# Kernel optimization log

Hardware: AMD Instinct MI355X
Metric: run time of the kernel (lower is better)

## Reference

```python
import jax, jax.numpy as jnp
import numpy as np

N = 100000      # nodes
E = 500000      # edges
F_IN = 165      # Elliptic feature dim
HID = 128       # hidden
HEADS = 2
DH = HID // HEADS  # 64, per-head GAT out dim
EPS = 1e-5


def setup_inputs() -> dict:
    key = jax.random.key(0)
    ks = jax.random.split(key, 40)

    def w(k, shape, fan_in):
        return (jax.random.normal(k, shape, jnp.float32) / np.sqrt(fan_in)).astype(jnp.float32)

    def bn_params(k, d):
        k1, k2 = jax.random.split(k)
        return (jnp.ones((d,), jnp.float32),                       # gamma
                jnp.zeros((d,), jnp.float32),                      # beta
                0.1 * jax.random.normal(k1, (d,), jnp.float32),    # running mean
                jax.random.uniform(k2, (d,), jnp.float32, 0.5, 1.5))  # running var

    bn1 = bn_params(ks[10], HID)
    bn2 = bn_params(ks[11], HID)
    bn3 = bn_params(ks[12], DH)

    return {
        "x": jax.random.normal(ks[0], (N, F_IN), jnp.float32),
        "edge_index": jax.random.randint(ks[1], (2, E), 0, N, jnp.int32),
        # input_proj
        "w_in": w(ks[2], (F_IN, HID), F_IN), "b_in": jnp.zeros((HID,), jnp.float32),
        # GCNConv
        "w_gcn": w(ks[3], (HID, HID), HID), "b_gcn": jnp.zeros((HID,), jnp.float32),
        "bn1_g": bn1[0], "bn1_b": bn1[1], "bn1_m": bn1[2], "bn1_v": bn1[3],
        # GATConv (heads=2, out=64, concat)
        "w_gat": w(ks[4], (HID, HEADS * DH), HID),
        "att_src": 0.1 * jax.random.normal(ks[5], (HEADS, DH), jnp.float32),
        "att_dst": 0.1 * jax.random.normal(ks[6], (HEADS, DH), jnp.float32),
        "b_gat": jnp.zeros((HEADS * DH,), jnp.float32),
        "bn2_g": bn2[0], "bn2_b": bn2[1], "bn2_m": bn2[2], "bn2_v": bn2[3],
        # SAGEConv (mean aggr)
        "w_sage_l": w(ks[7], (HID, DH), HID), "b_sage": jnp.zeros((DH,), jnp.float32),
        "w_sage_r": w(ks[8], (HID, DH), HID),
        "bn3_g": bn3[0], "bn3_b": bn3[1], "bn3_m": bn3[2], "bn3_v": bn3[3],
        # residual proj + classifier
        "w_res": w(ks[9], (HID, DH), HID), "b_res": jnp.zeros((DH,), jnp.float32),
        "w_c1": w(ks[13], (DH, 32), DH), "b_c1": jnp.zeros((32,), jnp.float32),
        "w_c2": w(ks[14], (32, 2), 32), "b_c2": jnp.zeros((2,), jnp.float32),
    }


def _bn(h, g, b, m, v):
    # eval-mode BatchNorm1d with running stats
    return (h - m) * (g / jnp.sqrt(v + EPS)) + b


def reference(x, edge_index, w_in, b_in, w_gcn, b_gcn,
              bn1_g, bn1_b, bn1_m, bn1_v,
              w_gat, att_src, att_dst, b_gat,
              bn2_g, bn2_b, bn2_m, bn2_v,
              w_sage_l, b_sage, w_sage_r,
              bn3_g, bn3_b, bn3_m, bn3_v,
              w_res, b_res, w_c1, b_c1, w_c2, b_c2):
    n = x.shape[0]
    src, dst = edge_index[0], edge_index[1]
    loop = jnp.arange(n, dtype=src.dtype)
    src_l = jnp.concatenate([src, loop])   # edges + self loops (GCN & GAT)
    dst_l = jnp.concatenate([dst, loop])

    # ---- input_proj (dropout = identity in eval) ----
    h = jax.nn.elu(x @ w_in + b_in)
    residual = h

    hw = h @ w_gcn
    deg = jax.ops.segment_sum(jnp.ones_like(dst_l, jnp.float32), dst_l, n)
    dinv = jnp.where(deg > 0, jax.lax.rsqrt(deg), 0.0)
    norm = dinv[src_l] * dinv[dst_l]                      # [E+N]
    h1 = jax.ops.segment_sum(hw[src_l] * norm[:, None], dst_l, n) + b_gcn
    h1 = jax.nn.elu(_bn(h1, bn1_g, bn1_b, bn1_m, bn1_v))

    # ---- GATConv (heads=2, concat, self loops, leaky_relu 0.2) ----
    g = (h1 @ w_gat).reshape(n, HEADS, DH)
    a_src = jnp.sum(g * att_src, axis=-1)                 # [N, H]
    a_dst = jnp.sum(g * att_dst, axis=-1)
    e = jax.nn.leaky_relu(a_src[src_l] + a_dst[dst_l], 0.2)   # [E+N, H]
    mx = jax.ops.segment_max(e, dst_l, n)                 # per-dst softmax max
    ex = jnp.exp(e - mx[dst_l])
    denom = jax.ops.segment_sum(ex, dst_l, n)
    alpha = ex / (denom[dst_l] + 1e-16)                   # [E+N, H]
    h2 = jax.ops.segment_sum(g[src_l] * alpha[:, :, None], dst_l, n)
    h2 = h2.reshape(n, HEADS * DH) + b_gat
    h2 = jax.nn.elu(_bn(h2, bn2_g, bn2_b, bn2_m, bn2_v))

    # ---- SAGEConv: W_l mean(neighbors) + W_r x + b (no self loops) ----
    deg_s = jax.ops.segment_sum(jnp.ones_like(dst, jnp.float32), dst, n)
    mean_nb = jax.ops.segment_sum(h2[src], dst, n) / jnp.maximum(deg_s, 1.0)[:, None]
    h3 = mean_nb @ w_sage_l + b_sage + h2 @ w_sage_r
    h3 = _bn(h3, bn3_g, bn3_b, bn3_m, bn3_v)
    h3 = jax.nn.elu(h3 + residual @ w_res + b_res)

    # ---- classifier ----
    z = jax.nn.elu(h3 @ w_c1 + b_c1)
    return z @ w_c2 + b_c2
```

## Files before the change

kernel.cpp:

```cpp
#include <hip/hip_runtime.h>
#include <cstdint>
#include <cstddef>

#define BN_EPS 1e-5f

typedef __attribute__((ext_vector_type(8))) short short8v;
typedef __attribute__((ext_vector_type(4))) float float4v;
typedef __attribute__((ext_vector_type(4))) unsigned int uint4v;
typedef unsigned int uint32;
typedef unsigned short ushort16;

__device__ __forceinline__ float elu_f(float v){ return v > 0.f ? v : expm1f(v); }
__device__ __forceinline__ float leaky_f(float v){ return v > 0.f ? v : 0.2f*v; }
__device__ __forceinline__ uint32 f2bf(float f){
  uint32 b = __float_as_uint(f);
  return (b + 0x7fffu + ((b >> 16) & 1u)) >> 16;
}
__device__ __forceinline__ float bflo(uint32 u){ return __uint_as_float(u << 16); }
__device__ __forceinline__ float bfhi(uint32 u){ return __uint_as_float(u & 0xffff0000u); }
__device__ __forceinline__ float readlane_f(float v, int l){
  return __int_as_float(__builtin_amdgcn_readlane(__float_as_int(v), l));
}
__device__ __forceinline__ uint32 fenc(float f){
  uint32 u = __float_as_uint(f);
  return (u >> 31) ? ~u : (u | 0x80000000u);
}
__device__ __forceinline__ float fdec(uint32 e){
  return (e & 0x80000000u) ? __uint_as_float(e & 0x7fffffffu) : __uint_as_float(~e);
}


__global__ void count_deg_kernel(const int* __restrict__ dst, int E, int* __restrict__ cnt){
  int i = blockIdx.x*blockDim.x + threadIdx.x;
  if(i < E) atomicAdd(&cnt[dst[i]], 1);
}

__global__ __launch_bounds__(1024) void scan_blocks(const int* __restrict__ cnt, int n,
                                                    int* __restrict__ part, int* __restrict__ bsum){
  __shared__ int wsum[16];
  int tid = threadIdx.x, lane = tid & 63, w = tid >> 6;
  int i = blockIdx.x*1024 + tid;
  int v = (i < n) ? cnt[i] : 0;
  int sv = v;
#pragma unroll
  for(int o = 1; o < 64; o <<= 1){
    int u = __shfl_up(sv, o);
    if(lane >= o) sv += u;
  }
  if(lane == 63) wsum[w] = sv;
  __syncthreads();
  int woff = 0;
#pragma unroll
  for(int q = 0; q < 16; q++) woff += (q < w) ? wsum[q] : 0;
  if(i < n) part[i] = woff + sv - v;
  if(tid == 1023) bsum[blockIdx.x] = woff + sv;
}

__global__ __launch_bounds__(1024) void scan_bsum(const int* __restrict__ bsum, int nb,
                                                  int* __restrict__ boff, int* __restrict__ rowptr, int n){
  __shared__ int wsum[16];
  int tid = threadIdx.x, lane = tid & 63, w = tid >> 6;
  int v = (tid < nb) ? bsum[tid] : 0;
  int sv = v;
#pragma unroll
  for(int o = 1; o < 64; o <<= 1){
    int u = __shfl_up(sv, o);
    if(lane >= o) sv += u;
  }
  if(lane == 63) wsum[w] = sv;
  __syncthreads();
  int woff = 0;
#pragma unroll
  for(int q = 0; q < 16; q++) woff += (q < w) ? wsum[q] : 0;
  if(tid < nb) boff[tid] = woff + sv - v;
  if(tid == 1023) rowptr[n] = woff + sv;
}

__global__ void scan_add_dinv(const int* __restrict__ part, const int* __restrict__ boff,
                              const int* __restrict__ cnt, int n,
                              int* __restrict__ rowptr, float* __restrict__ dinv){
  int i = blockIdx.x*blockDim.x + threadIdx.x;
  if(i < n){
    rowptr[i] = part[i] + boff[i >> 10];
    dinv[i] = rsqrtf((float)cnt[i] + 1.0f);
  }
}

__global__ void scatter_kernel(const int* __restrict__ src, const int* __restrict__ dst, int E,
                               const int* __restrict__ rowptr, int* __restrict__ fill,
                               int* __restrict__ col, int* __restrict__ pos){
  int i = blockIdx.x*blockDim.x + threadIdx.x;
  if(i < E){
    int s = src[i], d = dst[i];
    int p = rowptr[d] + atomicAdd(&fill[d], 1);
    col[p] = s;
    pos[i] = p;
  }
}


__global__ __launch_bounds__(256) void cvt_x(const float* __restrict__ x, uint2* __restrict__ xb, int total){
  int idx = blockIdx.x*256 + threadIdx.x;
  if(idx >= total) return;
  int row = idx/48;
  int cp = idx - row*48;
  int c = cp*4;
  const float* xr = x + (size_t)row*165;
  float v0 = (c   < 165) ? xr[c]   : 0.f;
  float v1 = (c+1 < 165) ? xr[c+1] : 0.f;
  float v2 = (c+2 < 165) ? xr[c+2] : 0.f;
  float v3 = (c+3 < 165) ? xr[c+3] : 0.f;
  xb[idx] = make_uint2(f2bf(v0) | (f2bf(v1) << 16), f2bf(v2) | (f2bf(v3) << 16));
}


__global__ void prep_scales(const float* __restrict__ bn1_g, const float* __restrict__ bn1_b,
    const float* __restrict__ bn1_m, const float* __restrict__ bn1_v, const float* __restrict__ b_gcn,
    const float* __restrict__ bn2_g, const float* __restrict__ bn2_b,
    const float* __restrict__ bn2_m, const float* __restrict__ bn2_v, const float* __restrict__ b_gat,
    const float* __restrict__ att_s, const float* __restrict__ att_d,
    const float* __restrict__ bn3_g, const float* __restrict__ bn3_b,
    const float* __restrict__ bn3_m, const float* __restrict__ bn3_v,
    const float* __restrict__ b_sage, const float* __restrict__ b_res,
    float* __restrict__ s1, float* __restrict__ b1c,
    float* __restrict__ s2, float* __restrict__ b2c,
    float* __restrict__ atts2, float* __restrict__ attd2,
    float* __restrict__ s3, float* __restrict__ bias3){
  int c = threadIdx.x;
  float v1 = bn1_g[c]*rsqrtf(bn1_v[c] + BN_EPS);
  s1[c] = v1;
  b1c[c] = (b_gcn[c] - bn1_m[c])*v1 + bn1_b[c];
  float v2 = bn2_g[c]*rsqrtf(bn2_v[c] + BN_EPS);
  s2[c] = v2;
  b2c[c] = (b_gat[c] - bn2_m[c])*v2 + bn2_b[c];
  atts2[c] = att_s[c]/v2;
  attd2[c] = att_d[c]/v2;
  if(c < 64){
    float v3 = bn3_g[c]*rsqrtf(bn3_v[c] + BN_EPS);
    s3[c] = v3;
    bias3[c] = (b_sage[c] - bn3_m[c])*v3 + bn3_b[c] + b_res[c];
  }
}


__device__ __forceinline__ void pack_region(const float* __restrict__ W, int K, int NOUT, int kbase, int idx,
                                            const float* __restrict__ scale, ushort16* __restrict__ out){
  int k = idx / NOUT, c = idx - k*NOUT;
  float v = (k < K) ? W[(size_t)k*NOUT + c] : 0.f;
  if(scale) v *= scale[c];
  int pk = kbase + k;
  out[(size_t)(pk >> 3)*NOUT*8 + (size_t)c*8 + (pk & 7)] = (ushort16)f2bf(v);
}

__global__ __launch_bounds__(256) void pack_all(const float* __restrict__ w_in, const float* __restrict__ w_gcn,
    const float* __restrict__ w_gat, const float* __restrict__ w_sl, const float* __restrict__ w_sr,
    const float* __restrict__ w_res,
    const float* __restrict__ s1, const float* __restrict__ s2, const float* __restrict__ s3,
    ushort16* __restrict__ pw_in, ushort16* __restrict__ pw_gcn,
    ushort16* __restrict__ pw_gat, ushort16* __restrict__ pw_cat){
  int b = blockIdx.x, t = threadIdx.x;
  if(b < 96)       pack_region(w_in,  165, 128, 0,   b*256 + t,        nullptr, pw_in);
  else if(b < 160) pack_region(w_gcn, 128, 128, 0,   (b-96)*256 + t,   s1,      pw_gcn);
  else if(b < 224) pack_region(w_gat, 128, 128, 0,   (b-160)*256 + t,  s2,      pw_gat);
  else if(b < 256) pack_region(w_sl,  128, 64,  0,   (b-224)*256 + t,  s3,      pw_cat);
  else if(b < 288) pack_region(w_sr,  128, 64,  128, (b-256)*256 + t,  s3,      pw_cat);
  else             pack_region(w_res, 128, 64,  256, (b-288)*256 + t,  nullptr, pw_cat);
}


template<int KSTEPS, int NOUT, int EPI>
__global__ __launch_bounds__(256) void mfma_gemm(
    const ushort16* __restrict__ A, int lda,
    const uint4v* __restrict__ pw,
    const float* __restrict__ bias,
    void* __restrict__ out, int ldo, int N,
    const float* __restrict__ dinv,
    const float* __restrict__ atts2, const float* __restrict__ attd2,
    float* __restrict__ a_src, float* __restrict__ a_dst,
    float* __restrict__ ess, uint32* __restrict__ Mint)
{
  constexpr int LDSV = KSTEPS*4*NOUT;
  __shared__ uint4v wlds[LDSV];
  int t = threadIdx.x;
#pragma unroll
  for(int q = 0; q < LDSV/256; q++)
    wlds[q*256 + t] = pw[q*256 + t];
  __syncthreads();

  int wid = t >> 6, lane = t & 63;
  int wm, wn;
  if(NOUT == 128){ wm = wid >> 1; wn = wid & 1; } else { wm = wid; wn = 0; }
  constexpr int MTILE = (NOUT == 128) ? 128 : 256;
  long row0 = (long)blockIdx.x*MTILE + wm*64;
  int l15 = lane & 15, lk = lane >> 4;
  int wn64 = wn*64;
  const ushort16* wl = (const ushort16*)wlds;

  float4v acc[4][4];
#pragma unroll
  for(int fm = 0; fm < 4; fm++)
#pragma unroll
    for(int fn = 0; fn < 4; fn++) acc[fm][fn] = (float4v){0.f,0.f,0.f,0.f};

  const ushort16* abase[4];
#pragma unroll
  for(int fm = 0; fm < 4; fm++){
    long r = row0 + fm*16 + l15;
    if(r > (long)N - 1) r = (long)N - 1;
    abase[fm] = A + r*(size_t)lda + lk*8;
  }

  short8v a[4];
#pragma unroll
  for(int fm = 0; fm < 4; fm++) a[fm] = *(const short8v*)(abase[fm]);

#pragma unroll
  for(int ks = 0; ks < KSTEPS; ks++){
    short8v b[4];
#pragma unroll
    for(int fn = 0; fn < 4; fn++){
      int c = wn64 + fn*16 + l15;
      b[fn] = *(const short8v*)(wl + ((size_t)((ks*4 + lk)*NOUT + c))*8);
    }
    short8v an[4];
    if(ks + 1 < KSTEPS){
#pragma unroll
      for(int fm = 0; fm < 4; fm++) an[fm] = *(const short8v*)(abase[fm] + (ks + 1)*32);
    }
#pragma unroll
    for(int fm = 0; fm < 4; fm++)
#pragma unroll
      for(int fn = 0; fn < 4; fn++)
        acc[fm][fn] = __builtin_amdgcn_mfma_f32_16x16x32_bf16(a[fm], b[fn], acc[fm][fn], 0, 0, 0);
    if(ks + 1 < KSTEPS){
#pragma unroll
      for(int fm = 0; fm < 4; fm++) a[fm] = an[fm];
    }
  }

#pragma unroll
  for(int fm = 0; fm < 4; fm++){
#pragma unroll
    for(int rr = 0; rr < 4; rr++){
      long r = row0 + fm*16 + lk*4 + rr;
      if(r < N){
        float dr = 0.f;
        if constexpr(EPI == 4) dr = dinv[r];
#pragma unroll
        for(int fn = 0; fn < 4; fn++){
          int c = wn64 + fn*16 + l15;
          float v = acc[fm][fn][rr];
          if constexpr(EPI == 1){ v += bias[c]; v = elu_f(v); }
          if constexpr(EPI == 4){ v *= dr; }
          ((ushort16*)out)[r*(size_t)ldo + c] = (ushort16)f2bf(v);
        }
      }
    }
  }

  if constexpr(EPI == 3){
    float as2[4], ad2[4];
#pragma unroll
    for(int fn = 0; fn < 4; fn++){
      int c = wn64 + fn*16 + l15;
      as2[fn] = atts2[c]; ad2[fn] = attd2[c];
    }
#pragma unroll
    for(int fm = 0; fm < 4; fm++){
#pragma unroll
      for(int rr = 0; rr < 4; rr++){
        float p1 = 0.f, p2 = 0.f;
#pragma unroll
        for(int fn = 0; fn < 4; fn++){
          p1 += acc[fm][fn][rr]*as2[fn];
          p2 += acc[fm][fn][rr]*ad2[fn];
        }
#pragma unroll
        for(int o = 1; o < 16; o <<= 1){
          p1 += __shfl_xor(p1, o);
          p2 += __shfl_xor(p2, o);
        }
        long r = row0 + fm*16 + lk*4 + rr;
        if(l15 == 0 && r < N){
          a_src[2*r + wn] = p1;
          a_dst[2*r + wn] = p2;
          float es = leaky_f(p1 + p2);
          ess[2*r + wn] = es;
          Mint[2*r + wn] = fenc(es);
        }
      }
    }
  }
}


__global__ __launch_bounds__(256) void gcn_agg(const uint32* __restrict__ hw2,
    const int* __restrict__ rowptr, const int* __restrict__ col,
    const float* __restrict__ dinv, const float* __restrict__ b1c,
    uint32* __restrict__ h1, int N)
{
  int t = threadIdx.x & 63;
  int w = __builtin_amdgcn_readfirstlane(threadIdx.x >> 6);
  float2 bc = ((const float2*)b1c)[t];
  int stride = gridDim.x*4;
  for(int i = blockIdx.x*4 + w; i < N; i += stride){
    int beg = rowptr[i], end = rowptr[i+1];
    float di = dinv[i];
    uint32 su = hw2[(size_t)i*64 + t];
    float a0 = bflo(su), a1 = bfhi(su);
#define GCN_ROW(q) { int row = __builtin_amdgcn_readlane(s, q); \
    uint32 u = hw2[(size_t)row*64 + t]; a0 += bflo(u); a1 += bfhi(u); }
    for(int c0 = beg; c0 < end; c0 += 64){
      int p = c0 + t;
      int cl = end - c0; if(cl > 64) cl = 64;
      int s = (p < end) ? col[p] : 0;
      int q = 0;
      for(; q + 4 <= cl; q += 4){ GCN_ROW(q) GCN_ROW(q+1) GCN_ROW(q+2) GCN_ROW(q+3) }
      for(; q < cl; q++){ GCN_ROW(q) }
    }
#undef GCN_ROW
    float v0 = a0*di + bc.x;
    float v1 = a1*di + bc.y;
    h1[(size_t)i*64 + t] = f2bf(elu_f(v0)) | (f2bf(elu_f(v1)) << 16);
  }
}


__global__ void edge_logit(const int* __restrict__ src, const int* __restrict__ dst,
                           const int* __restrict__ pos, int E,
                           const float* __restrict__ a_src, const float* __restrict__ a_dst,
                           float2* __restrict__ lcsr, uint32* __restrict__ Mint){
  int i = blockIdx.x*blockDim.x + threadIdx.x;
  if(i >= E) return;
  int s = src[i], d = dst[i], p = pos[i];
  float2 as = ((const float2*)a_src)[s];
  float2 ad = ((const float2*)a_dst)[d];
  float l0 = leaky_f(as.x + ad.x);
  float l1 = leaky_f(as.y + ad.y);
  lcsr[p] = make_float2(l0, l1);
  atomicMax(&Mint[2*d],   fenc(l0));
  atomicMax(&Mint[2*d+1], fenc(l1));
}


__global__ __launch_bounds__(256) void gat_gather(const uint32* __restrict__ g,
    const int* __restrict__ rowptr, const int* __restrict__ col,
    const float2* __restrict__ lcsr, const uint32* __restrict__ Mint, const float* __restrict__ ess,
    const float* __restrict__ b2c, uint32* __restrict__ h2out, int N)
{
  int t = threadIdx.x & 63;
  int w = __builtin_amdgcn_readfirstlane(threadIdx.x >> 6);
  float2 bc = ((const float2*)b2c)[t];
  int hl = t >> 5;
  int stride = gridDim.x*4;
  for(int i = blockIdx.x*4 + w; i < N; i += stride){
    int beg = rowptr[i], end = rowptr[i+1];
    float M0 = fdec(Mint[2*i]), M1 = fdec(Mint[2*i+1]);
    float es0 = ess[2*i], es1 = ess[2*i+1];
    float d0 = 0.f, d1 = 0.f, a0 = 0.f, a1 = 0.f;
#define GAT_ROW(q) { int row = __builtin_amdgcn_readlane(s, q); \
    float w0q = readlane_f(e0, q); \
    float w1q = readlane_f(e1, q); \
    float wq = hl ? w1q : w0q; \
    uint32 u = g[(size_t)row*64 + t]; a0 += wq*bflo(u); a1 += wq*bfhi(u); }
    for(int c0 = beg; c0 < end; c0 += 64){
      int p = c0 + t;
      int cl = end - c0; if(cl > 64) cl = 64;
      float e0 = 0.f, e1 = 0.f; int s = 0;
      if(p < end){
        float2 l = lcsr[p];
        e0 = __expf(l.x - M0); e1 = __expf(l.y - M1);
        s = col[p];
      }
      d0 += e0; d1 += e1;
      int q = 0;
      for(; q + 4 <= cl; q += 4){ GAT_ROW(q) GAT_ROW(q+1) GAT_ROW(q+2) GAT_ROW(q+3) }
      for(; q < cl; q++){ GAT_ROW(q) }
    }
#undef GAT_ROW
#pragma unroll
    for(int o = 32; o > 0; o >>= 1){ d0 += __shfl_xor(d0, o); d1 += __shfl_xor(d1, o); }
    float sw0 = __expf(es0 - M0), sw1 = __expf(es1 - M1);
    float rD = 1.f/(((hl ? d1 : d0) + (hl ? sw1 : sw0)) + 1e-16f);
    float sw = hl ? sw1 : sw0;
    uint32 su = g[(size_t)i*64 + t];
    float v0 = (a0 + sw*bflo(su))*rD + bc.x;
    float v1 = (a1 + sw*bfhi(su))*rD + bc.y;
    h2out[(size_t)i*192 + t] = f2bf(elu_f(v0)) | (f2bf(elu_f(v1)) << 16);
  }
}


__global__ __launch_bounds__(256) void sage_mean(const uint32* __restrict__ h2,
    const int* __restrict__ rowptr, const int* __restrict__ col,
    uint32* __restrict__ mout, int N)
{
  int t = threadIdx.x & 63;
  int w = __builtin_amdgcn_readfirstlane(threadIdx.x >> 6);
  int stride = gridDim.x*4;
  for(int i = blockIdx.x*4 + w; i < N; i += stride){
    int beg = rowptr[i], end = rowptr[i+1];
    float a0 = 0.f, a1 = 0.f;
#define SAGE_ROW(q) { int row = __builtin_amdgcn_readlane(s, q); \
    uint32 u = h2[(size_t)row*192 + t]; a0 += bflo(u); a1 += bfhi(u); }
    for(int c0 = beg; c0 < end; c0 += 64){
      int p = c0 + t;
      int cl = end - c0; if(cl > 64) cl = 64;
      int s = (p < end) ? col[p] : 0;
      int q = 0;
      for(; q + 4 <= cl; q += 4){ SAGE_ROW(q) SAGE_ROW(q+1) SAGE_ROW(q+2) SAGE_ROW(q+3) }
      for(; q < cl; q++){ SAGE_ROW(q) }
    }
#undef SAGE_ROW
    float inv = 1.f/fmaxf((float)(end - beg), 1.f);
    mout[(size_t)i*192 + t] = f2bf(a0*inv) | (f2bf(a1*inv) << 16);
  }
}


__global__ __launch_bounds__(256) void classifier_kernel(const uint32* __restrict__ h3,
    const float* __restrict__ w1, const float* __restrict__ b1,
    const float* __restrict__ w2, const float* __restrict__ b2,
    float* __restrict__ out, int N)
{
  __shared__ float hs[8][64];
  __shared__ float zs[8][32];
  int node0 = blockIdx.x*8;
  int t = threadIdx.x;
  {
    int r = t >> 5, cp = t & 31;
    int nd = node0 + r;
    uint32 u = (nd < N) ? h3[(size_t)nd*32 + cp] : 0u;
    hs[r][2*cp]   = bflo(u);
    hs[r][2*cp+1] = bfhi(u);
  }
  __syncthreads();
  int nn = t >> 5, ln = t & 31;
  float acc = b1[ln];
#pragma unroll
  for(int k = 0; k < 64; k++) acc += hs[nn][k]*w1[k*32 + ln];
  zs[nn][ln] = elu_f(acc);
  __syncthreads();
  int node = node0 + nn;
  if(ln < 2 && node < N){
    float o = b2[ln];
#pragma unroll
    for(int k = 0; k < 32; k++) o += zs[nn][k]*w2[k*2 + ln];
    out[(size_t)node*2 + ln] = o;
  }
}


extern "C" void kernel_launch(void* const* d_in, const int* in_sizes, int n_in,
                              void* d_out, int out_size, void* d_ws, size_t ws_size,
                              hipStream_t stream)
{
  (void)n_in; (void)out_size; (void)ws_size;
  const float* x      = (const float*)d_in[0];
  const int*   ei     = (const int*)  d_in[1];
  const float* w_in   = (const float*)d_in[2];
  const float* b_in   = (const float*)d_in[3];
  const float* w_gcn  = (const float*)d_in[4];
  const float* b_gcn  = (const float*)d_in[5];
  const float* bn1_g  = (const float*)d_in[6];
  const float* bn1_b  = (const float*)d_in[7];
  const float* bn1_m  = (const float*)d_in[8];
  const float* bn1_v  = (const float*)d_in[9];
  const float* w_gat  = (const float*)d_in[10];
  const float* att_s  = (const float*)d_in[11];
  const float* att_d  = (const float*)d_in[12];
  const float* b_gat  = (const float*)d_in[13];
  const float* bn2_g  = (const float*)d_in[14];
  const float* bn2_b  = (const float*)d_in[15];
  const float* bn2_m  = (const float*)d_in[16];
  const float* bn2_v  = (const float*)d_in[17];
  const float* w_sl   = (const float*)d_in[18];
  const float* b_sage = (const float*)d_in[19];
  const float* w_sr   = (const float*)d_in[20];
  const float* bn3_g  = (const float*)d_in[21];
  const float* bn3_b  = (const float*)d_in[22];
  const float* bn3_m  = (const float*)d_in[23];
  const float* bn3_v  = (const float*)d_in[24];
  const float* w_res  = (const float*)d_in[25];
  const float* b_res  = (const float*)d_in[26];
  const float* w_c1   = (const float*)d_in[27];
  const float* b_c1   = (const float*)d_in[28];
  const float* w_c2   = (const float*)d_in[29];
  const float* b_c2   = (const float*)d_in[30];

  const int F_IN = 165;
  int N = in_sizes[0]/F_IN;
  int E = in_sizes[1]/2;
  const int* srcp = ei;
  const int* dstp = ei + E;
  int nb = (N + 1023) >> 10;

  char* p = (char*)d_ws;
  auto alloc = [&](size_t bytes) -> char* {
    char* q = p; p += (bytes + 255) & ~(size_t)255; return q;
  };
  ushort16* Acat  = (ushort16*)alloc((size_t)N*384*2);
  ushort16* xb    = (ushort16*)alloc((size_t)N*192*2);
  ushort16* bufG  = (ushort16*)alloc((size_t)N*128*2);
  float* a_src    = (float*)alloc((size_t)N*2*4);
  float* a_dst    = (float*)alloc((size_t)N*2*4);
  float* ess      = (float*)alloc((size_t)N*2*4);
  uint32* Mint    = (uint32*)alloc((size_t)N*2*4);
  float* dinv     = (float*)alloc((size_t)N*4);
  int* cnt        = (int*)alloc((size_t)N*4);
  int* fill       = (int*)alloc((size_t)N*4);
  int* rowptr     = (int*)alloc((size_t)(N+1)*4);
  int* part       = (int*)alloc((size_t)N*4);
  int* bsum       = (int*)alloc(1024*4);
  int* boff       = (int*)alloc(1024*4);
  int* col        = (int*)alloc((size_t)E*4);
  int* pos        = (int*)alloc((size_t)E*4);
  float2* lcsr    = (float2*)alloc((size_t)E*8);
  float* s1       = (float*)alloc(128*4);
  float* b1c      = (float*)alloc(128*4);
  float* s2       = (float*)alloc(128*4);
  float* b2c      = (float*)alloc(128*4);
  float* atts2    = (float*)alloc(128*4);
  float* attd2    = (float*)alloc(128*4);
  float* s3       = (float*)alloc(64*4);
  float* bias3    = (float*)alloc(64*4);
  ushort16* pw_in  = (ushort16*)alloc(6*4*128*16);
  ushort16* pw_gcn = (ushort16*)alloc(4*4*128*16);
  ushort16* pw_gat = (ushort16*)alloc(4*4*128*16);
  ushort16* pw_cat = (ushort16*)alloc(12*4*64*16);

  ushort16* h1 = xb;
  ushort16* h3 = bufG;

  hipMemsetAsync(cnt, 0, (size_t)((char*)(fill + N) - (char*)cnt), stream);

  count_deg_kernel<<<(E+255)/256, 256, 0, stream>>>(dstp, E, cnt);
  scan_blocks<<<nb, 1024, 0, stream>>>(cnt, N, part, bsum);
  scan_bsum<<<1, 1024, 0, stream>>>(bsum, nb, boff, rowptr, N);
  scan_add_dinv<<<(N+255)/256, 256, 0, stream>>>(part, boff, cnt, N, rowptr, dinv);
  scatter_kernel<<<(E+255)/256, 256, 0, stream>>>(srcp, dstp, E, rowptr, fill, col, pos);

  cvt_x<<<(N*48 + 255)/256, 256, 0, stream>>>(x, (uint2*)xb, N*48);
  prep_scales<<<1, 128, 0, stream>>>(bn1_g, bn1_b, bn1_m, bn1_v, b_gcn,
                                     bn2_g, bn2_b, bn2_m, bn2_v, b_gat,
                                     att_s, att_d,
                                     bn3_g, bn3_b, bn3_m, bn3_v, b_sage, b_res,
                                     s1, b1c, s2, b2c, atts2, attd2, s3, bias3);
  pack_all<<<320, 256, 0, stream>>>(w_in, w_gcn, w_gat, w_sl, w_sr, w_res,
                                    s1, s2, s3, pw_in, pw_gcn, pw_gat, pw_cat);

  int g128 = (N + 127)/128;
  int g256 = (N + 255)/256;
  int gagg = (N + 3)/4; if(gagg > 4096) gagg = 4096;

  mfma_gemm<6,128,1><<<g128, 256, 0, stream>>>(xb, 192, (const uint4v*)pw_in, b_in,
      (void*)(Acat + 256), 384, N, nullptr, nullptr, nullptr, nullptr, nullptr, nullptr, nullptr);
  mfma_gemm<4,128,4><<<g128, 256, 0, stream>>>(Acat + 256, 384, (const uint4v*)pw_gcn, nullptr,
      (void*)bufG, 128, N, dinv, nullptr, nullptr, nullptr, nullptr, nullptr, nullptr);
  gcn_agg<<<gagg, 256, 0, stream>>>((const uint32*)bufG, rowptr, col, dinv, b1c,
                                    (uint32*)h1, N);
  mfma_gemm<4,128,3><<<g128, 256, 0, stream>>>(h1, 128, (const uint4v*)pw_gat, nullptr,
      (void*)bufG, 128, N, nullptr, atts2, attd2, a_src, a_dst, ess, Mint);
  edge_logit<<<(E+255)/256, 256, 0, stream>>>(srcp, dstp, pos, E, a_src, a_dst, lcsr, Mint);
  gat_gather<<<gagg, 256, 0, stream>>>((const uint32*)bufG, rowptr, col, lcsr, Mint, ess,
                                       b2c, (uint32*)Acat + 64, N);
  sage_mean<<<gagg, 256, 0, stream>>>((const uint32*)Acat + 64, rowptr, col, (uint32*)Acat, N);
  mfma_gemm<12,64,1><<<g256, 256, 0, stream>>>(Acat, 384, (const uint4v*)pw_cat, bias3,
      (void*)h3, 64, N, nullptr, nullptr, nullptr, nullptr, nullptr, nullptr, nullptr);
  classifier_kernel<<<(N+7)/8, 256, 0, stream>>>((const uint32*)h3, w_c1, b_c1, w_c2, b_c2,
                                                 (float*)d_out, N);
}
```

Measured before the change: 378.3 us.

## Fuse GAT edge logits and softmax max into the gather kernel

Removes the separate edge_logit kernel, along with its pos/lcsr buffers and the atomicMax on encoded per-node maxima. The gather kernel now computes leaky-relu logits per edge from a_src/a_dst and takes the softmax max with a wave-level shuffle reduction. Rows with degree up to 64 do this in one pass. Larger rows make a second pass over col and a_src to recompute the logits. This saves an E-sized kernel launch, its scattered writes and its atomics, and the scatter kernel no longer writes pos, at the cost of extra gathers of a_src inside the aggregation.

```diff
diff --git a/kernel.cpp b/kernel.cpp
--- a/kernel.cpp
+++ b/kernel.cpp
@@ -20,13 +20,6 @@
 __device__ __forceinline__ float bfhi(uint32 u){ return __uint_as_float(u & 0xffff0000u); }
 __device__ __forceinline__ float readlane_f(float v, int l){
   return __int_as_float(__builtin_amdgcn_readlane(__float_as_int(v), l));
-}
-__device__ __forceinline__ uint32 fenc(float f){
-  uint32 u = __float_as_uint(f);
-  return (u >> 31) ? ~u : (u | 0x80000000u);
-}
-__device__ __forceinline__ float fdec(uint32 e){
-  return (e & 0x80000000u) ? __uint_as_float(e & 0x7fffffffu) : __uint_as_float(~e);
 }
 
 
@@ -88,13 +81,12 @@
 
 __global__ void scatter_kernel(const int* __restrict__ src, const int* __restrict__ dst, int E,
                                const int* __restrict__ rowptr, int* __restrict__ fill,
-                               int* __restrict__ col, int* __restrict__ pos){
+                               int* __restrict__ col){
   int i = blockIdx.x*blockDim.x + threadIdx.x;
   if(i < E){
     int s = src[i], d = dst[i];
     int p = rowptr[d] + atomicAdd(&fill[d], 1);
     col[p] = s;
-    pos[i] = p;
   }
 }
 
@@ -177,7 +169,7 @@
     const float* __restrict__ dinv,
     const float* __restrict__ atts2, const float* __restrict__ attd2,
     float* __restrict__ a_src, float* __restrict__ a_dst,
-    float* __restrict__ ess, uint32* __restrict__ Mint)
+    float* __restrict__ ess)
 {
   constexpr int LDSV = KSTEPS*4*NOUT;
   __shared__ uint4v wlds[LDSV];
@@ -284,9 +276,7 @@
         if(l15 == 0 && r < N){
           a_src[2*r + wn] = p1;
           a_dst[2*r + wn] = p2;
-          float es = leaky_f(p1 + p2);
-          ess[2*r + wn] = es;
-          Mint[2*r + wn] = fenc(es);
+          ess[2*r + wn] = leaky_f(p1 + p2);
         }
       }
     }
@@ -326,27 +316,11 @@
 }
 
 
-__global__ void edge_logit(const int* __restrict__ src, const int* __restrict__ dst,
-                           const int* __restrict__ pos, int E,
-                           const float* __restrict__ a_src, const float* __restrict__ a_dst,
-                           float2* __restrict__ lcsr, uint32* __restrict__ Mint){
-  int i = blockIdx.x*blockDim.x + threadIdx.x;
-  if(i >= E) return;
-  int s = src[i], d = dst[i], p = pos[i];
-  float2 as = ((const float2*)a_src)[s];
-  float2 ad = ((const float2*)a_dst)[d];
-  float l0 = leaky_f(as.x + ad.x);
-  float l1 = leaky_f(as.y + ad.y);
-  lcsr[p] = make_float2(l0, l1);
-  atomicMax(&Mint[2*d],   fenc(l0));
-  atomicMax(&Mint[2*d+1], fenc(l1));
-}
-
-
 __global__ __launch_bounds__(256) void gat_gather(const uint32* __restrict__ g,
     const int* __restrict__ rowptr, const int* __restrict__ col,
-    const float2* __restrict__ lcsr, const uint32* __restrict__ Mint, const float* __restrict__ ess,
-    const float* __restrict__ b2c, uint32* __restrict__ h2out, int N)
+    const float* __restrict__ a_src, const float* __restrict__ a_dst,
+    const float* __restrict__ ess, const float* __restrict__ b2c,
+    uint32* __restrict__ h2out, int N)
 {
   int t = threadIdx.x & 63;
   int w = __builtin_amdgcn_readfirstlane(threadIdx.x >> 6);
@@ -355,29 +329,62 @@
   int stride = gridDim.x*4;
   for(int i = blockIdx.x*4 + w; i < N; i += stride){
     int beg = rowptr[i], end = rowptr[i+1];
-    float M0 = fdec(Mint[2*i]), M1 = fdec(Mint[2*i+1]);
+    int deg = end - beg;
+    float2 ad = ((const float2*)a_dst)[i];
     float es0 = ess[2*i], es1 = ess[2*i+1];
     float d0 = 0.f, d1 = 0.f, a0 = 0.f, a1 = 0.f;
-#define GAT_ROW(q) { int row = __builtin_amdgcn_readlane(s, q); \
+    float M0, M1;
+#define GAT_ROWF(q) { int row = __builtin_amdgcn_readlane(s, q); \
     float w0q = readlane_f(e0, q); \
     float w1q = readlane_f(e1, q); \
     float wq = hl ? w1q : w0q; \
     uint32 u = g[(size_t)row*64 + t]; a0 += wq*bflo(u); a1 += wq*bfhi(u); }
-    for(int c0 = beg; c0 < end; c0 += 64){
-      int p = c0 + t;
-      int cl = end - c0; if(cl > 64) cl = 64;
-      float e0 = 0.f, e1 = 0.f; int s = 0;
+    if(deg <= 64){
+      int p = beg + t;
+      int s = 0; float l0 = -3e38f, l1 = -3e38f;
       if(p < end){
-        float2 l = lcsr[p];
-        e0 = __expf(l.x - M0); e1 = __expf(l.y - M1);
         s = col[p];
+        float2 as = ((const float2*)a_src)[s];
+        l0 = leaky_f(as.x + ad.x);
+        l1 = leaky_f(as.y + ad.y);
       }
-      d0 += e0; d1 += e1;
+      float m0 = fmaxf(l0, es0), m1 = fmaxf(l1, es1);
+#pragma unroll
+      for(int o = 32; o > 0; o >>= 1){ m0 = fmaxf(m0, __shfl_xor(m0, o)); m1 = fmaxf(m1, __shfl_xor(m1, o)); }
+      M0 = m0; M1 = m1;
+      float e0 = (p < end) ? __expf(l0 - M0) : 0.f;
+      float e1 = (p < end) ? __expf(l1 - M1) : 0.f;
+      d0 = e0; d1 = e1;
       int q = 0;
-      for(; q + 4 <= cl; q += 4){ GAT_ROW(q) GAT_ROW(q+1) GAT_ROW(q+2) GAT_ROW(q+3) }
-      for(; q < cl; q++){ GAT_ROW(q) }
-    }
-#undef GAT_ROW
+      for(; q + 4 <= deg; q += 4){ GAT_ROWF(q) GAT_ROWF(q+1) GAT_ROWF(q+2) GAT_ROWF(q+3) }
+      for(; q < deg; q++){ GAT_ROWF(q) }
+    } else {
+      float m0 = es0, m1 = es1;
+      for(int p = beg + t; p < end; p += 64){
+        float2 as = ((const float2*)a_src)[col[p]];
+        m0 = fmaxf(m0, leaky_f(as.x + ad.x));
+        m1 = fmaxf(m1, leaky_f(as.y + ad.y));
+      }
+#pragma unroll
+      for(int o = 32; o > 0; o >>= 1){ m0 = fmaxf(m0, __shfl_xor(m0, o)); m1 = fmaxf(m1, __shfl_xor(m1, o)); }
+      M0 = m0; M1 = m1;
+      for(int c0 = beg; c0 < end; c0 += 64){
+        int p = c0 + t;
+        int cl = end - c0; if(cl > 64) cl = 64;
+        float e0 = 0.f, e1 = 0.f; int s = 0;
+        if(p < end){
+          s = col[p];
+          float2 as = ((const float2*)a_src)[s];
+          e0 = __expf(leaky_f(as.x + ad.x) - M0);
+          e1 = __expf(leaky_f(as.y + ad.y) - M1);
+        }
+        d0 += e0; d1 += e1;
+        int q = 0;
+        for(; q + 4 <= cl; q += 4){ GAT_ROWF(q) GAT_ROWF(q+1) GAT_ROWF(q+2) GAT_ROWF(q+3) }
+        for(; q < cl; q++){ GAT_ROWF(q) }
+      }
+    }
+#undef GAT_ROWF
 #pragma unroll
     for(int o = 32; o > 0; o >>= 1){ d0 += __shfl_xor(d0, o); d1 += __shfl_xor(d1, o); }
     float sw0 = __expf(es0 - M0), sw1 = __expf(es1 - M1);
@@ -505,7 +512,6 @@
   float* a_src    = (float*)alloc((size_t)N*2*4);
   float* a_dst    = (float*)alloc((size_t)N*2*4);
   float* ess      = (float*)alloc((size_t)N*2*4);
-  uint32* Mint    = (uint32*)alloc((size_t)N*2*4);
   float* dinv     = (float*)alloc((size_t)N*4);
   int* cnt        = (int*)alloc((size_t)N*4);
   int* fill       = (int*)alloc((size_t)N*4);
@@ -514,8 +520,6 @@
   int* bsum       = (int*)alloc(1024*4);
   int* boff       = (int*)alloc(1024*4);
   int* col        = (int*)alloc((size_t)E*4);
-  int* pos        = (int*)alloc((size_t)E*4);
-  float2* lcsr    = (float2*)alloc((size_t)E*8);
   float* s1       = (float*)alloc(128*4);
   float* b1c      = (float*)alloc(128*4);
   float* s2       = (float*)alloc(128*4);
@@ -538,7 +542,7 @@
   scan_blocks<<<nb, 1024, 0, stream>>>(cnt, N, part, bsum);
   scan_bsum<<<1, 1024, 0, stream>>>(bsum, nb, boff, rowptr, N);
   scan_add_dinv<<<(N+255)/256, 256, 0, stream>>>(part, boff, cnt, N, rowptr, dinv);
-  scatter_kernel<<<(E+255)/256, 256, 0, stream>>>(srcp, dstp, E, rowptr, fill, col, pos);
+  scatter_kernel<<<(E+255)/256, 256, 0, stream>>>(srcp, dstp, E, rowptr, fill, col);
 
   cvt_x<<<(N*48 + 255)/256, 256, 0, stream>>>(x, (uint2*)xb, N*48);
   prep_scales<<<1, 128, 0, stream>>>(bn1_g, bn1_b, bn1_m, bn1_v, b_gcn,
@@ -554,19 +558,18 @@
   int gagg = (N + 3)/4; if(gagg > 4096) gagg = 4096;
 
   mfma_gemm<6,128,1><<<g128, 256, 0, stream>>>(xb, 192, (const uint4v*)pw_in, b_in,
-      (void*)(Acat + 256), 384, N, nullptr, nullptr, nullptr, nullptr, nullptr, nullptr, nullptr);
+      (void*)(Acat + 256), 384, N, nullptr, nullptr, nullptr, nullptr, nullptr, nullptr);
   mfma_gemm<4,128,4><<<g128, 256, 0, stream>>>(Acat + 256, 384, (const uint4v*)pw_gcn, nullptr,
-      (void*)bufG, 128, N, dinv, nullptr, nullptr, nullptr, nullptr, nullptr, nullptr);
+      (void*)bufG, 128, N, dinv, nullptr, nullptr, nullptr, nullptr, nullptr);
   gcn_agg<<<gagg, 256, 0, stream>>>((const uint32*)bufG, rowptr, col, dinv, b1c,
                                     (uint32*)h1, N);
   mfma_gemm<4,128,3><<<g128, 256, 0, stream>>>(h1, 128, (const uint4v*)pw_gat, nullptr,
-      (void*)bufG, 128, N, nullptr, atts2, attd2, a_src, a_dst, ess, Mint);
-  edge_logit<<<(E+255)/256, 256, 0, stream>>>(srcp, dstp, pos, E, a_src, a_dst, lcsr, Mint);
-  gat_gather<<<gagg, 256, 0, stream>>>((const uint32*)bufG, rowptr, col, lcsr, Mint, ess,
+      (void*)bufG, 128, N, nullptr, atts2, attd2, a_src, a_dst, ess);
+  gat_gather<<<gagg, 256, 0, stream>>>((const uint32*)bufG, rowptr, col, a_src, a_dst, ess,
                                        b2c, (uint32*)Acat + 64, N);
   sage_mean<<<gagg, 256, 0, stream>>>((const uint32*)Acat + 64, rowptr, col, (uint32*)Acat, N);
   mfma_gemm<12,64,1><<<g256, 256, 0, stream>>>(Acat, 384, (const uint4v*)pw_cat, bias3,
-      (void*)h3, 64, N, nullptr, nullptr, nullptr, nullptr, nullptr, nullptr, nullptr);
+      (void*)h3, 64, N, nullptr, nullptr, nullptr, nullptr, nullptr, nullptr);
   classifier_kernel<<<(N+7)/8, 256, 0, stream>>>((const uint32*)h3, w_c1, b_c1, w_c2, b_c2,
                                                  (float*)d_out, N);
 }
```

New measurement: 336.8 us. -11.0%, faster.
